# Performance work log

Hardware: AMD Instinct MI355X
Metric: run time of the kernel (lower is better)

## Reference

```python
import jax, jax.numpy as jnp
import numpy as np

N = 100000   # nodes
E = 1600000  # edges
C = 128      # d_model
F = 6        # LIFT_FEATURES
L = 2        # num_gcn_layers
EPS = 1e-5

def _gelu(v):
    return jax.nn.gelu(v, approximate=False)  # torch nn.GELU() default = exact erf

def setup_inputs() -> dict:
    key = jax.random.key(0)
    ks = jax.random.split(key, 24)
    def w(k, shape):
        fan_in = shape[-2] if len(shape) >= 2 else shape[-1]
        return (jax.random.normal(k, shape, jnp.float32) / np.sqrt(fan_in)).astype(jnp.float32)
    inp = {
        "x": jax.random.normal(ks[0], (1, N, 9), jnp.float32),
        "edge_index": jax.random.randint(ks[1], (2, E), 0, N, jnp.int32),
        "edge_values": jax.random.uniform(ks[2], (E,), jnp.float32),
        # lift MLP
        "lift_w1": w(ks[3], (F, C)), "lift_b1": jnp.zeros((C,), jnp.float32),
        "lift_w2": w(ks[4], (C, C)), "lift_b2": jnp.zeros((C,), jnp.float32),
        # GCN layer params stacked over L layers
        "self_w": w(ks[5], (L, C, C)),  "self_b": jnp.zeros((L, C), jnp.float32),
        "neigh_w": w(ks[6], (L, C, C)), "neigh_b": jnp.zeros((L, C), jnp.float32),
        "gate_w1": w(ks[7], (L, 2 * C, C)), "gate_b1": jnp.zeros((L, C), jnp.float32),
        "gate_w2": w(ks[8], (L, C, C)),     "gate_b2": jnp.zeros((L, C), jnp.float32),
        # final LayerNorm
        "norm_g": jnp.ones((C,), jnp.float32), "norm_b": jnp.zeros((C,), jnp.float32),
    }
    return inp

def reference(x, edge_index, edge_values,
              lift_w1, lift_b1, lift_w2, lift_b2,
              self_w, self_b, neigh_w, neigh_b,
              gate_w1, gate_b1, gate_w2, gate_b2,
              norm_g, norm_b):
    # node_feats = x[..., 3:], B == 1 path -> work on [N, F]
    nf = x[0, :, 3:]
    h = _gelu(nf @ lift_w1 + lift_b1) @ lift_w2 + lift_b2  # [N, C]
    row, col = edge_index[0], edge_index[1]
    for l in range(L):
        neighbor = h @ neigh_w[l] + neigh_b[l]                 # [N, C]
        messages = neighbor[col] * edge_values[:, None]        # gather + weight [E, C]
        aggr = jnp.zeros_like(h).at[row].add(messages)         # scatter-add [N, C]
        self_f = h @ self_w[l] + self_b[l]                     # [N, C]
        u = jnp.concatenate([self_f, aggr], axis=-1)           # [N, 2C]
        u = _gelu(u @ gate_w1[l] + gate_b1[l]) @ gate_w2[l] + gate_b2[l]
        h = h + u
    mu = jnp.mean(h, axis=-1, keepdims=True)
    var = jnp.mean(jnp.square(h - mu), axis=-1, keepdims=True)
    h = (h - mu) * jax.lax.rsqrt(var + EPS) * norm_g + norm_b
    return h[None]  # [1, N, C]
```

## Files before the change

### kernel.cpp

```cpp
#include <hip/hip_runtime.h>
#include <math.h>

#define C 128

typedef unsigned short u16;
typedef __attribute__((ext_vector_type(8))) short short8;
typedef __attribute__((ext_vector_type(4))) float f32x4;

__device__ __forceinline__ float gelu_f(float v) {
    return 0.5f * v * (1.0f + erff(v * 0.70710678118654752f));
}

__device__ __forceinline__ u16 f2bf(float f) {
    unsigned u = __float_as_uint(f);
    unsigned r = (u + 0x7fffu + ((u >> 16) & 1u)) >> 16;
    return (u16)r;
}
__device__ __forceinline__ float b2f(u16 u) {
    return __uint_as_float(((unsigned)u) << 16);
}

__device__ __forceinline__ void g2lds16(const void* g, void* l) {
    __builtin_amdgcn_global_load_lds(
        (const __attribute__((address_space(1))) unsigned int*)g,
        (__attribute__((address_space(3))) unsigned int*)l, 16, 0, 0);
}

__global__ void prep_weights_kernel(const float* __restrict__ self_w,
                                    const float* __restrict__ self_b,
                                    const float* __restrict__ gate_w1,
                                    const float* __restrict__ gate_b1,
                                    float* __restrict__ Wc, float* __restrict__ bc) {
    const int l = blockIdx.y;
    const int i = blockIdx.x;
    const int j = threadIdx.x;
    const float* gw = gate_w1 + l * 256 * C;
    if (i < C) {
        const float* sw = self_w + l * C * C + i * C;
        float s = 0.f;
        for (int k = 0; k < C; ++k) s += sw[k] * gw[k * C + j];
        Wc[l * C * C + i * C + j] = s;
    } else {
        const float* sb = self_b + l * C;
        float s = gate_b1[l * C + j];
        for (int k = 0; k < C; ++k) s += sb[k] * gw[k * C + j];
        bc[l * C + j] = s;
    }
}

__global__ void wsplit_kernel(const float* __restrict__ lw2, const float* __restrict__ nw,
                              const float* __restrict__ gw1, const float* __restrict__ gw2,
                              const float* __restrict__ Wc,
                              u16* __restrict__ wh, u16* __restrict__ wl) {
    const int col = blockIdx.x;
    const int mat = blockIdx.y;
    const int k = threadIdx.x;
    const float* src;
    if (mat == 0)      src = lw2;
    else if (mat <= 2) src = nw + (size_t)(mat - 1) * 16384;
    else if (mat <= 4) src = gw1 + (size_t)(mat - 3) * 32768 + 16384;
    else if (mat <= 6) src = gw2 + (size_t)(mat - 5) * 16384;
    else               src = Wc + (size_t)(mat - 7) * 16384;
    float v = src[k * C + col];
    u16 hi = f2bf(v);
    size_t di = (size_t)mat * 16384 + (size_t)col * C + k;
    wh[di] = hi;
    wl[di] = f2bf(v - b2f(hi));
}

__global__ void lift_hidden_kernel(const float* __restrict__ x,
                                   const float* __restrict__ w1,
                                   const float* __restrict__ b1,
                                   u16* __restrict__ oh, u16* __restrict__ ol, int N) {
    int idx = blockIdx.x * 256 + threadIdx.x;
    if (idx >= N * C) return;
    int n = idx >> 7, c = idx & 127;
    const float* xr = x + n * 9 + 3;
    float s = b1[c];
#pragma unroll
    for (int f = 0; f < 6; ++f) s += xr[f] * w1[f * C + c];
    s = gelu_f(s);
    u16 hi = f2bf(s);
    oh[idx] = hi;
    ol[idx] = f2bf(s - b2f(hi));
}

__global__ __launch_bounds__(256, 2)
void gemm_mfma_kernel(const u16* __restrict__ A0h, const u16* __restrict__ A0l,
                      const u16* __restrict__ W0h, const u16* __restrict__ W0l,
                      const u16* __restrict__ A1h, const u16* __restrict__ A1l,
                      const u16* __restrict__ W1h, const u16* __restrict__ W1l,
                      const float* __restrict__ bias,
                      const u16* __restrict__ Rh, const u16* __restrict__ Rl,
                      u16* __restrict__ Oh, u16* __restrict__ Ol,
                      int M, int nsrc, int act) {
    __shared__ u16 lds[4][128 * 64];
    const int t = threadIdx.x;
    const int l = t & 63;
    const int w = t >> 6;
    const int wr = w >> 1, wc = w & 1;
    const int m0 = blockIdx.x * 128;
    const int kg = l >> 4;
    const int swz = l & 7;
    const int l15 = l & 15;

    f32x4 acc[4][4];
#pragma unroll
    for (int m = 0; m < 4; ++m)
#pragma unroll
        for (int n = 0; n < 4; ++n) acc[m][n] = (f32x4)(0.f);

    for (int sidx = 0; sidx < nsrc; ++sidx) {
        const u16* Ah = sidx ? A1h : A0h;
        const u16* Al = sidx ? A1l : A0l;
        const u16* Wh = sidx ? W1h : W0h;
        const u16* Wl = sidx ? W1l : W0l;
        for (int kh = 0; kh < 2; ++kh) {
            const u16* gp[4] = {Ah, Al, Wh, Wl};
#pragma unroll
            for (int p = 0; p < 4; ++p) {
#pragma unroll
                for (int it = 0; it < 4; ++it) {
                    int chunk = it * 256 + t;
                    int row = chunk >> 3;
                    int cl = (chunk & 7) ^ (row & 7);
                    int grow = (p < 2) ? ((m0 + row < M) ? m0 + row : M - 1) : row;
                    const u16* src = gp[p] + (size_t)grow * C + kh * 64 + cl * 8;
                    g2lds16(src, &lds[p][chunk * 8]);
                }
            }
            __syncthreads();
#pragma unroll
            for (int s = 0; s < 2; ++s) {
                const int ci = ((s * 4 + kg) ^ swz) * 16;
                short8 ah[4], al[4], bh[4], bl[4];
#pragma unroll
                for (int m = 0; m < 4; ++m) {
                    int ro = (wr * 64 + m * 16 + l15) * 128;
                    ah[m] = *(const short8*)((const char*)&lds[0][0] + ro + ci);
                    al[m] = *(const short8*)((const char*)&lds[1][0] + ro + ci);
                }
#pragma unroll
                for (int n = 0; n < 4; ++n) {
                    int ro = (wc * 64 + n * 16 + l15) * 128;
                    bh[n] = *(const short8*)((const char*)&lds[2][0] + ro + ci);
                    bl[n] = *(const short8*)((const char*)&lds[3][0] + ro + ci);
                }
#pragma unroll
                for (int m = 0; m < 4; ++m)
#pragma unroll
                    for (int n = 0; n < 4; ++n)
                        acc[m][n] = __builtin_amdgcn_mfma_f32_16x16x32_bf16(ah[m], bh[n], acc[m][n], 0, 0, 0);
#pragma unroll
                for (int m = 0; m < 4; ++m)
#pragma unroll
                    for (int n = 0; n < 4; ++n)
                        acc[m][n] = __builtin_amdgcn_mfma_f32_16x16x32_bf16(al[m], bh[n], acc[m][n], 0, 0, 0);
#pragma unroll
                for (int m = 0; m < 4; ++m)
#pragma unroll
                    for (int n = 0; n < 4; ++n)
                        acc[m][n] = __builtin_amdgcn_mfma_f32_16x16x32_bf16(ah[m], bl[n], acc[m][n], 0, 0, 0);
            }
            __syncthreads();
        }
    }

    float bj[4];
#pragma unroll
    for (int n = 0; n < 4; ++n) bj[n] = bias[wc * 64 + n * 16 + l15];
#pragma unroll
    for (int m = 0; m < 4; ++m) {
#pragma unroll
        for (int r = 0; r < 4; ++r) {
            int row = m0 + wr * 64 + m * 16 + kg * 4 + r;
            if (row < M) {
#pragma unroll
                for (int n = 0; n < 4; ++n) {
                    int col = wc * 64 + n * 16 + l15;
                    float o = acc[m][n][r] + bj[n];
                    if (act) o = gelu_f(o);
                    size_t idx = (size_t)row * C + col;
                    if (Rh) o += b2f(Rh[idx]) + b2f(Rl[idx]);
                    u16 hi = f2bf(o);
                    Oh[idx] = hi;
                    Ol[idx] = f2bf(o - b2f(hi));
                }
            }
        }
    }
}

__global__ void zero_i32_kernel(int* __restrict__ p, int n) {
    int i = blockIdx.x * 256 + threadIdx.x;
    if (i < n) p[i] = 0;
}

__global__ void deg_count_kernel(const int* __restrict__ row, int* __restrict__ deg, int E) {
    int e = blockIdx.x * 256 + threadIdx.x;
    if (e < E) atomicAdd(&deg[row[e]], 1);
}

__global__ void scan_chunk_kernel(const int* __restrict__ deg, int* __restrict__ offs,
                                  int* __restrict__ part, int N) {
    __shared__ int ts[256];
    const int t = threadIdx.x;
    const int base = blockIdx.x * 1024 + t * 4;
    int v0 = (base + 0 < N) ? deg[base + 0] : 0;
    int v1 = (base + 1 < N) ? deg[base + 1] : 0;
    int v2 = (base + 2 < N) ? deg[base + 2] : 0;
    int v3 = (base + 3 < N) ? deg[base + 3] : 0;
    int l0 = v0, l1 = l0 + v1, l2 = l1 + v2, l3 = l2 + v3;
    ts[t] = l3;
    __syncthreads();
    for (int d = 1; d < 256; d <<= 1) {
        int add = (t >= d) ? ts[t - d] : 0;
        __syncthreads();
        ts[t] += add;
        __syncthreads();
    }
    int tex = ts[t] - l3;
    if (base + 0 < N) offs[base + 1] = tex + l0;
    if (base + 1 < N) offs[base + 2] = tex + l1;
    if (base + 2 < N) offs[base + 3] = tex + l2;
    if (base + 3 < N) offs[base + 4] = tex + l3;
    if (t == 255) part[blockIdx.x] = ts[255];
}

__global__ void scan_partials_kernel(int* __restrict__ part, int n) {
    __shared__ int s[128];
    const int t = threadIdx.x;
    int v = (t < n) ? part[t] : 0;
    s[t] = v;
    __syncthreads();
    for (int d = 1; d < 128; d <<= 1) {
        int add = (t >= d) ? s[t - d] : 0;
        __syncthreads();
        s[t] += add;
        __syncthreads();
    }
    if (t < n) part[t] = s[t] - v;
}

__global__ void scan_add_kernel(int* __restrict__ offs, const int* __restrict__ part,
                                int* __restrict__ cursor, int N) {
    const int t = threadIdx.x;
    const int base = blockIdx.x * 1024 + t * 4;
    const int add = part[blockIdx.x];
#pragma unroll
    for (int j = 0; j < 4; ++j) {
        int i = base + j;
        if (i < N) {
            int v = offs[i + 1] + add;
            offs[i + 1] = v;
            if (i + 1 < N) cursor[i + 1] = v;
        }
    }
    if (blockIdx.x == 0 && t == 0) {
        offs[0] = 0;
        cursor[0] = 0;
    }
}

__global__ void fill_kernel(const int* __restrict__ row, const int* __restrict__ col,
                            const float* __restrict__ ev, int* __restrict__ cursor,
                            int2* __restrict__ epack, int E) {
    int e = blockIdx.x * 256 + threadIdx.x;
    if (e >= E) return;
    int r = row[e];
    int pos = atomicAdd(&cursor[r], 1);
    int2 p;
    p.x = col[e];
    p.y = __float_as_int(ev[e]);
    epack[pos] = p;
}

__global__ __launch_bounds__(256)
void aggregate_kernel(const u16* __restrict__ nh, const u16* __restrict__ nl,
                      const int* __restrict__ offs, const int2* __restrict__ epack,
                      u16* __restrict__ oh, u16* __restrict__ ol, int N) {
    const int lane = threadIdx.x & 63;
    const int node = (blockIdx.x << 2) + (threadIdx.x >> 6);
    if (node >= N) return;
    const int s = offs[node], e = offs[node + 1];
    const int ch = lane << 1;
    float ax = 0.f, ay = 0.f, bx = 0.f, by = 0.f;
    int i = s;
    for (; i + 2 <= e; i += 2) {
        int2 p0 = epack[i];
        int2 p1 = epack[i + 1];
        float v0 = __int_as_float(p0.y);
        float v1 = __int_as_float(p1.y);
        ushort2 h0 = *(const ushort2*)&nh[(size_t)p0.x * C + ch];
        ushort2 l0 = *(const ushort2*)&nl[(size_t)p0.x * C + ch];
        ushort2 h1 = *(const ushort2*)&nh[(size_t)p1.x * C + ch];
        ushort2 l1 = *(const ushort2*)&nl[(size_t)p1.x * C + ch];
        ax += v0 * (b2f(h0.x) + b2f(l0.x));
        ay += v0 * (b2f(h0.y) + b2f(l0.y));
        bx += v1 * (b2f(h1.x) + b2f(l1.x));
        by += v1 * (b2f(h1.y) + b2f(l1.y));
    }
    if (i < e) {
        int2 p = epack[i];
        float v = __int_as_float(p.y);
        ushort2 h0 = *(const ushort2*)&nh[(size_t)p.x * C + ch];
        ushort2 l0 = *(const ushort2*)&nl[(size_t)p.x * C + ch];
        ax += v * (b2f(h0.x) + b2f(l0.x));
        ay += v * (b2f(h0.y) + b2f(l0.y));
    }
    float sx = ax + bx, sy = ay + by;
    ushort2 ho, lo;
    ho.x = f2bf(sx); ho.y = f2bf(sy);
    lo.x = f2bf(sx - b2f(ho.x)); lo.y = f2bf(sy - b2f(ho.y));
    size_t idx = (size_t)node * C + ch;
    *(ushort2*)&oh[idx] = ho;
    *(ushort2*)&ol[idx] = lo;
}

__global__ __launch_bounds__(256)
void layernorm_kernel(const u16* __restrict__ hh, const u16* __restrict__ hl,
                      const float* __restrict__ g, const float* __restrict__ b,
                      float* __restrict__ out, int N) {
    const int lane = threadIdx.x & 63;
    const int node = (blockIdx.x << 2) + (threadIdx.x >> 6);
    if (node >= N) return;
    size_t idx = (size_t)node * C + (lane << 1);
    ushort2 vh = *(const ushort2*)&hh[idx];
    ushort2 vl = *(const ushort2*)&hl[idx];
    float vx = b2f(vh.x) + b2f(vl.x);
    float vy = b2f(vh.y) + b2f(vl.y);
    float s = vx + vy;
#pragma unroll
    for (int m = 1; m < 64; m <<= 1) s += __shfl_xor(s, m, 64);
    float mu = s * (1.f / 128.f);
    float dx = vx - mu, dy = vy - mu;
    float q = dx * dx + dy * dy;
#pragma unroll
    for (int m = 1; m < 64; m <<= 1) q += __shfl_xor(q, m, 64);
    float rs = 1.f / sqrtf(q * (1.f / 128.f) + 1e-5f);
    float2 gg = *(const float2*)&g[lane << 1];
    float2 bb = *(const float2*)&b[lane << 1];
    float2 o;
    o.x = dx * rs * gg.x + bb.x;
    o.y = dy * rs * gg.y + bb.y;
    *(float2*)&out[idx] = o;
}

extern "C" void kernel_launch(void* const* d_in, const int* in_sizes, int n_in,
                              void* d_out, int out_size, void* d_ws, size_t ws_size,
                              hipStream_t stream) {
    const float* x    = (const float*)d_in[0];
    const int*   ei   = (const int*)d_in[1];
    const float* ev   = (const float*)d_in[2];
    const float* lw1  = (const float*)d_in[3];
    const float* lb1  = (const float*)d_in[4];
    const float* lw2  = (const float*)d_in[5];
    const float* lb2  = (const float*)d_in[6];
    const float* sw   = (const float*)d_in[7];
    const float* sb   = (const float*)d_in[8];
    const float* nw   = (const float*)d_in[9];
    const float* nbi  = (const float*)d_in[10];
    const float* gw1  = (const float*)d_in[11];
    const float* gb1  = (const float*)d_in[12];
    const float* gw2  = (const float*)d_in[13];
    const float* gb2  = (const float*)d_in[14];
    const float* ng   = (const float*)d_in[15];
    const float* nbt  = (const float*)d_in[16];

    const int N = in_sizes[0] / 9;
    const int E = in_sizes[2];
    const int L = in_sizes[7] / (C * C);
    const int* row = ei;
    const int* col = ei + E;

    float* out = (float*)d_out;

    char* p = (char*)d_ws;
    u16* Hh = (u16*)p; p += (size_t)N * C * 2;
    u16* Hl = (u16*)p; p += (size_t)N * C * 2;
    u16* Bh = (u16*)p; p += (size_t)N * C * 2;
    u16* Bl = (u16*)p; p += (size_t)N * C * 2;
    u16* Ch = (u16*)p; p += (size_t)N * C * 2;
    u16* Cl = (u16*)p; p += (size_t)N * C * 2;
    int2* epack = (int2*)p; p += (size_t)E * sizeof(int2);
    float* Wc = (float*)p; p += (size_t)L * C * C * sizeof(float);
    float* bc = (float*)p; p += (size_t)L * C * sizeof(float);
    u16* wh = (u16*)p; p += (size_t)9 * C * C * 2;
    u16* wl = (u16*)p; p += (size_t)9 * C * C * 2;
    int* deg    = (int*)p; p += (size_t)N * sizeof(int);
    int* offs   = (int*)p; p += (size_t)(N + 1) * sizeof(int);
    int* cursor = (int*)p; p += (size_t)N * sizeof(int);
    int* part   = (int*)p; p += 1024 * sizeof(int);

    const int NB_SCAN = (N + 1023) / 1024;
    const int GB_NODE = (N + 3) / 4;
    const int GB_EDGE = (E + 255) / 256;
    const int GB_GEMM = (N + 127) / 128;

    prep_weights_kernel<<<dim3(C + 1, L), C, 0, stream>>>(sw, sb, gw1, gb1, Wc, bc);
    wsplit_kernel<<<dim3(C, 9), C, 0, stream>>>(lw2, nw, gw1, gw2, Wc, wh, wl);

    lift_hidden_kernel<<<(N * C + 255) / 256, 256, 0, stream>>>(x, lw1, lb1, Bh, Bl, N);
    gemm_mfma_kernel<<<GB_GEMM, 256, 0, stream>>>(
        Bh, Bl, wh, wl, nullptr, nullptr, nullptr, nullptr,
        lb2, nullptr, nullptr, Hh, Hl, N, 1, 0);

    zero_i32_kernel<<<(N + 255) / 256, 256, 0, stream>>>(deg, N);
    deg_count_kernel<<<GB_EDGE, 256, 0, stream>>>(row, deg, E);
    scan_chunk_kernel<<<NB_SCAN, 256, 0, stream>>>(deg, offs, part, N);
    scan_partials_kernel<<<1, 128, 0, stream>>>(part, NB_SCAN);
    scan_add_kernel<<<NB_SCAN, 256, 0, stream>>>(offs, part, cursor, N);
    fill_kernel<<<GB_EDGE, 256, 0, stream>>>(row, col, ev, cursor, epack, E);

    for (int l = 0; l < L; ++l) {
        const u16* nwh  = wh + (size_t)(1 + l) * 16384;
        const u16* nwl_ = wl + (size_t)(1 + l) * 16384;
        const u16* g1h  = wh + (size_t)(3 + l) * 16384;
        const u16* g1l  = wl + (size_t)(3 + l) * 16384;
        const u16* g2h  = wh + (size_t)(5 + l) * 16384;
        const u16* g2l  = wl + (size_t)(5 + l) * 16384;
        const u16* wch  = wh + (size_t)(7 + l) * 16384;
        const u16* wcl  = wl + (size_t)(7 + l) * 16384;

        gemm_mfma_kernel<<<GB_GEMM, 256, 0, stream>>>(
            Hh, Hl, nwh, nwl_, nullptr, nullptr, nullptr, nullptr,
            nbi + (size_t)l * C, nullptr, nullptr, Bh, Bl, N, 1, 0);
        aggregate_kernel<<<GB_NODE, 256, 0, stream>>>(Bh, Bl, offs, epack, Ch, Cl, N);
        gemm_mfma_kernel<<<GB_GEMM, 256, 0, stream>>>(
            Hh, Hl, wch, wcl, Ch, Cl, g1h, g1l,
            bc + (size_t)l * C, nullptr, nullptr, Bh, Bl, N, 2, 1);
        gemm_mfma_kernel<<<GB_GEMM, 256, 0, stream>>>(
            Bh, Bl, g2h, g2l, nullptr, nullptr, nullptr, nullptr,
            gb2 + (size_t)l * C, Hh, Hl, Hh, Hl, N, 1, 0);
    }

    layernorm_kernel<<<GB_NODE, 256, 0, stream>>>(Hh, Hl, ng, nbt, out, N);
}
```

Measured before the change: 853.8 us.

## Fold neighbor projection into gate weights and fuse final LayerNorm into GEMM

Uses linearity to aggregate raw h first, then folds neigh_w into gate_w1's aggregate half (precomputed Wn1). The neighbor bias is applied through per-node edge-value sums times a folded bias vector. This removes one N×C×C GEMM per layer and its intermediate round trip. The final LayerNorm moves into the last GEMM's epilogue through an LDS tile, which drops a separate kernel and the read-back of h. LDS grows slightly to 128×132 floats, and the order of rounding changes.

```diff
diff --git a/kernel.cpp b/kernel.cpp
--- a/kernel.cpp
+++ b/kernel.cpp
@@ -28,39 +28,58 @@
 
 __global__ void prep_weights_kernel(const float* __restrict__ self_w,
                                     const float* __restrict__ self_b,
+                                    const float* __restrict__ neigh_w,
+                                    const float* __restrict__ neigh_b,
                                     const float* __restrict__ gate_w1,
                                     const float* __restrict__ gate_b1,
-                                    float* __restrict__ Wc, float* __restrict__ bc) {
-    const int l = blockIdx.y;
+                                    float* __restrict__ Wc, float* __restrict__ bc,
+                                    float* __restrict__ Wn1, float* __restrict__ bv,
+                                    int L_) {
+    const int y = blockIdx.y;
     const int i = blockIdx.x;
     const int j = threadIdx.x;
-    const float* gw = gate_w1 + l * 256 * C;
-    if (i < C) {
-        const float* sw = self_w + l * C * C + i * C;
-        float s = 0.f;
-        for (int k = 0; k < C; ++k) s += sw[k] * gw[k * C + j];
-        Wc[l * C * C + i * C + j] = s;
+    if (y < L_) {
+        const int l = y;
+        const float* gw = gate_w1 + (size_t)l * 256 * C;
+        if (i < C) {
+            const float* swr = self_w + (size_t)l * C * C + (size_t)i * C;
+            float s = 0.f;
+            for (int k = 0; k < C; ++k) s += swr[k] * gw[k * C + j];
+            Wc[(size_t)l * C * C + (size_t)i * C + j] = s;
+        } else {
+            const float* sbr = self_b + (size_t)l * C;
+            float s = gate_b1[(size_t)l * C + j];
+            for (int k = 0; k < C; ++k) s += sbr[k] * gw[k * C + j];
+            bc[(size_t)l * C + j] = s;
+        }
     } else {
-        const float* sb = self_b + l * C;
-        float s = gate_b1[l * C + j];
-        for (int k = 0; k < C; ++k) s += sb[k] * gw[k * C + j];
-        bc[l * C + j] = s;
-    }
-}
-
-__global__ void wsplit_kernel(const float* __restrict__ lw2, const float* __restrict__ nw,
-                              const float* __restrict__ gw1, const float* __restrict__ gw2,
-                              const float* __restrict__ Wc,
+        const int l = y - L_;
+        const float* gw = gate_w1 + (size_t)l * 256 * C + (size_t)C * C;
+        if (i < C) {
+            const float* nwr = neigh_w + (size_t)l * C * C + (size_t)i * C;
+            float s = 0.f;
+            for (int k = 0; k < C; ++k) s += nwr[k] * gw[k * C + j];
+            Wn1[(size_t)l * C * C + (size_t)i * C + j] = s;
+        } else {
+            const float* nbr = neigh_b + (size_t)l * C;
+            float s = 0.f;
+            for (int k = 0; k < C; ++k) s += nbr[k] * gw[k * C + j];
+            bv[(size_t)l * C + j] = s;
+        }
+    }
+}
+
+__global__ void wsplit_kernel(const float* __restrict__ lw2, const float* __restrict__ gw2,
+                              const float* __restrict__ Wc, const float* __restrict__ Wn1,
                               u16* __restrict__ wh, u16* __restrict__ wl) {
     const int col = blockIdx.x;
     const int mat = blockIdx.y;
     const int k = threadIdx.x;
     const float* src;
     if (mat == 0)      src = lw2;
-    else if (mat <= 2) src = nw + (size_t)(mat - 1) * 16384;
-    else if (mat <= 4) src = gw1 + (size_t)(mat - 3) * 32768 + 16384;
-    else if (mat <= 6) src = gw2 + (size_t)(mat - 5) * 16384;
-    else               src = Wc + (size_t)(mat - 7) * 16384;
+    else if (mat <= 2) src = gw2 + (size_t)(mat - 1) * 16384;
+    else if (mat <= 4) src = Wc + (size_t)(mat - 3) * 16384;
+    else               src = Wn1 + (size_t)(mat - 5) * 16384;
     float v = src[k * C + col];
     u16 hi = f2bf(v);
     size_t di = (size_t)mat * 16384 + (size_t)col * C + k;
@@ -91,10 +110,15 @@
                       const u16* __restrict__ A1h, const u16* __restrict__ A1l,
                       const u16* __restrict__ W1h, const u16* __restrict__ W1l,
                       const float* __restrict__ bias,
+                      const float* __restrict__ bias2,
+                      const float* __restrict__ rowscale,
                       const u16* __restrict__ Rh, const u16* __restrict__ Rl,
                       u16* __restrict__ Oh, u16* __restrict__ Ol,
+                      const float* __restrict__ lng, const float* __restrict__ lnb,
+                      float* __restrict__ outF,
                       int M, int nsrc, int act) {
-    __shared__ u16 lds[4][128 * 64];
+    __shared__ __align__(16) char smem[128 * 132 * 4];
+    u16* lds0 = (u16*)smem;
     const int t = threadIdx.x;
     const int l = t & 63;
     const int w = t >> 6;
@@ -126,7 +150,7 @@
                     int cl = (chunk & 7) ^ (row & 7);
                     int grow = (p < 2) ? ((m0 + row < M) ? m0 + row : M - 1) : row;
                     const u16* src = gp[p] + (size_t)grow * C + kh * 64 + cl * 8;
-                    g2lds16(src, &lds[p][chunk * 8]);
+                    g2lds16(src, lds0 + (size_t)p * 8192 + chunk * 8);
                 }
             }
             __syncthreads();
@@ -137,14 +161,14 @@
 #pragma unroll
                 for (int m = 0; m < 4; ++m) {
                     int ro = (wr * 64 + m * 16 + l15) * 128;
-                    ah[m] = *(const short8*)((const char*)&lds[0][0] + ro + ci);
-                    al[m] = *(const short8*)((const char*)&lds[1][0] + ro + ci);
+                    ah[m] = *(const short8*)((const char*)lds0 + ro + ci);
+                    al[m] = *(const short8*)((const char*)lds0 + 16384 + ro + ci);
                 }
 #pragma unroll
                 for (int n = 0; n < 4; ++n) {
                     int ro = (wc * 64 + n * 16 + l15) * 128;
-                    bh[n] = *(const short8*)((const char*)&lds[2][0] + ro + ci);
-                    bl[n] = *(const short8*)((const char*)&lds[3][0] + ro + ci);
+                    bh[n] = *(const short8*)((const char*)lds0 + 32768 + ro + ci);
+                    bl[n] = *(const short8*)((const char*)lds0 + 49152 + ro + ci);
                 }
 #pragma unroll
                 for (int m = 0; m < 4; ++m)
@@ -166,27 +190,62 @@
         }
     }
 
-    float bj[4];
-#pragma unroll
-    for (int n = 0; n < 4; ++n) bj[n] = bias[wc * 64 + n * 16 + l15];
+    float* lnt = (float*)smem;
+    float bj[4], b2j[4];
+#pragma unroll
+    for (int n = 0; n < 4; ++n) {
+        bj[n] = bias[wc * 64 + n * 16 + l15];
+        b2j[n] = bias2 ? bias2[wc * 64 + n * 16 + l15] : 0.f;
+    }
 #pragma unroll
     for (int m = 0; m < 4; ++m) {
 #pragma unroll
         for (int r = 0; r < 4; ++r) {
-            int row = m0 + wr * 64 + m * 16 + kg * 4 + r;
-            if (row < M) {
-#pragma unroll
-                for (int n = 0; n < 4; ++n) {
-                    int col = wc * 64 + n * 16 + l15;
-                    float o = acc[m][n][r] + bj[n];
-                    if (act) o = gelu_f(o);
-                    size_t idx = (size_t)row * C + col;
-                    if (Rh) o += b2f(Rh[idx]) + b2f(Rl[idx]);
+            int rowl = wr * 64 + m * 16 + kg * 4 + r;
+            int grow = m0 + rowl;
+            bool ok = grow < M;
+            float rs_ = (bias2 && ok) ? rowscale[grow] : 0.f;
+#pragma unroll
+            for (int n = 0; n < 4; ++n) {
+                int col = wc * 64 + n * 16 + l15;
+                float o = acc[m][n][r] + bj[n];
+                if (bias2) o += rs_ * b2j[n];
+                if (act) o = gelu_f(o);
+                size_t idx = (size_t)grow * C + col;
+                if (Rh && ok) o += b2f(Rh[idx]) + b2f(Rl[idx]);
+                if (outF) {
+                    lnt[rowl * 132 + col] = o;
+                } else if (ok) {
                     u16 hi = f2bf(o);
                     Oh[idx] = hi;
                     Ol[idx] = f2bf(o - b2f(hi));
                 }
             }
+        }
+    }
+
+    if (outF) {
+        __syncthreads();
+        float2 gg = *(const float2*)&lng[l << 1];
+        float2 bb = *(const float2*)&lnb[l << 1];
+        for (int r = 0; r < 32; ++r) {
+            int rowl = w * 32 + r;
+            int grow = m0 + rowl;
+            if (grow >= M) break;
+            float2 v = *(const float2*)&lnt[rowl * 132 + (l << 1)];
+            float s = v.x + v.y;
+#pragma unroll
+            for (int mk = 1; mk < 64; mk <<= 1) s += __shfl_xor(s, mk, 64);
+            float mu = s * (1.f / 128.f);
+            float dx = v.x - mu, dy = v.y - mu;
+            float q = dx * dx + dy * dy;
+#pragma unroll
+            for (int mk = 1; mk < 64; mk <<= 1) q += __shfl_xor(q, mk, 64);
+            float rsq = 1.f / sqrtf(q * (1.f / 128.f) + 1e-5f);
+            float2 o;
+            o.x = dx * rsq * gg.x + bb.x;
+            o.y = dy * rsq * gg.y + bb.y;
+            *(float2*)&outF[(size_t)grow * C + (l << 1)] = o;
         }
     }
 }
@@ -278,13 +337,14 @@
 __global__ __launch_bounds__(256)
 void aggregate_kernel(const u16* __restrict__ nh, const u16* __restrict__ nl,
                       const int* __restrict__ offs, const int2* __restrict__ epack,
-                      u16* __restrict__ oh, u16* __restrict__ ol, int N) {
+                      u16* __restrict__ oh, u16* __restrict__ ol,
+                      float* __restrict__ sumev, int N) {
     const int lane = threadIdx.x & 63;
     const int node = (blockIdx.x << 2) + (threadIdx.x >> 6);
     if (node >= N) return;
     const int s = offs[node], e = offs[node + 1];
     const int ch = lane << 1;
-    float ax = 0.f, ay = 0.f, bx = 0.f, by = 0.f;
+    float ax = 0.f, ay = 0.f, bx = 0.f, by = 0.f, ssum = 0.f;
     int i = s;
     for (; i + 2 <= e; i += 2) {
         int2 p0 = epack[i];
@@ -299,6 +359,7 @@
         ay += v0 * (b2f(h0.y) + b2f(l0.y));
         bx += v1 * (b2f(h1.x) + b2f(l1.x));
         by += v1 * (b2f(h1.y) + b2f(l1.y));
+        ssum += v0 + v1;
     }
     if (i < e) {
         int2 p = epack[i];
@@ -307,6 +368,7 @@
         ushort2 l0 = *(const ushort2*)&nl[(size_t)p.x * C + ch];
         ax += v * (b2f(h0.x) + b2f(l0.x));
         ay += v * (b2f(h0.y) + b2f(l0.y));
+        ssum += v;
     }
     float sx = ax + bx, sy = ay + by;
     ushort2 ho, lo;
@@ -315,35 +377,7 @@
     size_t idx = (size_t)node * C + ch;
     *(ushort2*)&oh[idx] = ho;
     *(ushort2*)&ol[idx] = lo;
-}
-
-__global__ __launch_bounds__(256)
-void layernorm_kernel(const u16* __restrict__ hh, const u16* __restrict__ hl,
-                      const float* __restrict__ g, const float* __restrict__ b,
-                      float* __restrict__ out, int N) {
-    const int lane = threadIdx.x & 63;
-    const int node = (blockIdx.x << 2) + (threadIdx.x >> 6);
-    if (node >= N) return;
-    size_t idx = (size_t)node * C + (lane << 1);
-    ushort2 vh = *(const ushort2*)&hh[idx];
-    ushort2 vl = *(const ushort2*)&hl[idx];
-    float vx = b2f(vh.x) + b2f(vl.x);
-    float vy = b2f(vh.y) + b2f(vl.y);
-    float s = vx + vy;
-#pragma unroll
-    for (int m = 1; m < 64; m <<= 1) s += __shfl_xor(s, m, 64);
-    float mu = s * (1.f / 128.f);
-    float dx = vx - mu, dy = vy - mu;
-    float q = dx * dx + dy * dy;
-#pragma unroll
-    for (int m = 1; m < 64; m <<= 1) q += __shfl_xor(q, m, 64);
-    float rs = 1.f / sqrtf(q * (1.f / 128.f) + 1e-5f);
-    float2 gg = *(const float2*)&g[lane << 1];
-    float2 bb = *(const float2*)&b[lane << 1];
-    float2 o;
-    o.x = dx * rs * gg.x + bb.x;
-    o.y = dy * rs * gg.y + bb.y;
-    *(float2*)&out[idx] = o;
+    if (lane == 0) sumev[node] = ssum;
 }
 
 extern "C" void kernel_launch(void* const* d_in, const int* in_sizes, int n_in,
@@ -383,10 +417,13 @@
     u16* Ch = (u16*)p; p += (size_t)N * C * 2;
     u16* Cl = (u16*)p; p += (size_t)N * C * 2;
     int2* epack = (int2*)p; p += (size_t)E * sizeof(int2);
-    float* Wc = (float*)p; p += (size_t)L * C * C * sizeof(float);
-    float* bc = (float*)p; p += (size_t)L * C * sizeof(float);
-    u16* wh = (u16*)p; p += (size_t)9 * C * C * 2;
-    u16* wl = (u16*)p; p += (size_t)9 * C * C * 2;
+    float* Wc  = (float*)p; p += (size_t)L * C * C * sizeof(float);
+    float* Wn1 = (float*)p; p += (size_t)L * C * C * sizeof(float);
+    float* bc  = (float*)p; p += (size_t)L * C * sizeof(float);
+    float* bv  = (float*)p; p += (size_t)L * C * sizeof(float);
+    float* sumev = (float*)p; p += (size_t)N * sizeof(float);
+    u16* wh = (u16*)p; p += (size_t)7 * C * C * 2;
+    u16* wl = (u16*)p; p += (size_t)7 * C * C * 2;
     int* deg    = (int*)p; p += (size_t)N * sizeof(int);
     int* offs   = (int*)p; p += (size_t)(N + 1) * sizeof(int);
     int* cursor = (int*)p; p += (size_t)N * sizeof(int);
@@ -397,13 +434,15 @@
     const int GB_EDGE = (E + 255) / 256;
     const int GB_GEMM = (N + 127) / 128;
 
-    prep_weights_kernel<<<dim3(C + 1, L), C, 0, stream>>>(sw, sb, gw1, gb1, Wc, bc);
-    wsplit_kernel<<<dim3(C, 9), C, 0, stream>>>(lw2, nw, gw1, gw2, Wc, wh, wl);
+    prep_weights_kernel<<<dim3(C + 1, 2 * L), C, 0, stream>>>(
+        sw, sb, nw, nbi, gw1, gb1, Wc, bc, Wn1, bv, L);
+    wsplit_kernel<<<dim3(C, 7), C, 0, stream>>>(lw2, gw2, Wc, Wn1, wh, wl);
 
     lift_hidden_kernel<<<(N * C + 255) / 256, 256, 0, stream>>>(x, lw1, lb1, Bh, Bl, N);
     gemm_mfma_kernel<<<GB_GEMM, 256, 0, stream>>>(
         Bh, Bl, wh, wl, nullptr, nullptr, nullptr, nullptr,
-        lb2, nullptr, nullptr, Hh, Hl, N, 1, 0);
+        lb2, nullptr, nullptr, nullptr, nullptr, Hh, Hl,
+        nullptr, nullptr, nullptr, N, 1, 0);
 
     zero_i32_kernel<<<(N + 255) / 256, 256, 0, stream>>>(deg, N);
     deg_count_kernel<<<GB_EDGE, 256, 0, stream>>>(row, deg, E);
@@ -413,26 +452,26 @@
     fill_kernel<<<GB_EDGE, 256, 0, stream>>>(row, col, ev, cursor, epack, E);
 
     for (int l = 0; l < L; ++l) {
-        const u16* nwh  = wh + (size_t)(1 + l) * 16384;
-        const u16* nwl_ = wl + (size_t)(1 + l) * 16384;
-        const u16* g1h  = wh + (size_t)(3 + l) * 16384;
-        const u16* g1l  = wl + (size_t)(3 + l) * 16384;
-        const u16* g2h  = wh + (size_t)(5 + l) * 16384;
-        const u16* g2l  = wl + (size_t)(5 + l) * 16384;
-        const u16* wch  = wh + (size_t)(7 + l) * 16384;
-        const u16* wcl  = wl + (size_t)(7 + l) * 16384;
-
+        const u16* g2h = wh + (size_t)(1 + l) * 16384;
+        const u16* g2l = wl + (size_t)(1 + l) * 16384;
+        const u16* wch = wh + (size_t)(3 + l) * 16384;
+        const u16* wcl = wl + (size_t)(3 + l) * 16384;
+        const u16* n1h = wh + (size_t)(5 + l) * 16384;
+        const u16* n1l = wl + (size_t)(5 + l) * 16384;
+        const bool last = (l == L - 1);
+
+        aggregate_kernel<<<GB_NODE, 256, 0, stream>>>(Hh, Hl, offs, epack, Ch, Cl, sumev, N);
         gemm_mfma_kernel<<<GB_GEMM, 256, 0, stream>>>(
-            Hh, Hl, nwh, nwl_, nullptr, nullptr, nullptr, nullptr,
-            nbi + (size_t)l * C, nullptr, nullptr, Bh, Bl, N, 1, 0);
-        aggregate_kernel<<<GB_NODE, 256, 0, stream>>>(Bh, Bl, offs, epack, Ch, Cl, N);
-        gemm_mfma_kernel<<<GB_GEMM, 256, 0, stream>>>(
-            Hh, Hl, wch, wcl, Ch, Cl, g1h, g1l,
-            bc + (size_t)l * C, nullptr, nullptr, Bh, Bl, N, 2, 1);
+            Hh, Hl, wch, wcl, Ch, Cl, n1h, n1l,
+            bc + (size_t)l * C, bv + (size_t)l * C, sumev,
+            nullptr, nullptr, Bh, Bl,
+            nullptr, nullptr, nullptr, N, 2, 1);
         gemm_mfma_kernel<<<GB_GEMM, 256, 0, stream>>>(
             Bh, Bl, g2h, g2l, nullptr, nullptr, nullptr, nullptr,
-            gb2 + (size_t)l * C, Hh, Hl, Hh, Hl, N, 1, 0);
-    }
-
-    layernorm_kernel<<<GB_NODE, 256, 0, stream>>>(Hh, Hl, ng, nbt, out, N);
-}
+            gb2 + (size_t)l * C, nullptr, nullptr,
+            Hh, Hl,
+            last ? nullptr : Hh, last ? nullptr : Hl,
+            last ? ng : nullptr, last ? nbt : nullptr, last ? out : nullptr,
+            N, 1, 0);
+    }
+}
```

Result: no change. 870.2 us (+1.9%).
